# Kernel tuning notes

Hardware: AMD Instinct MI355X
Metric: run time of the kernel (lower is better)

Reference implementation:

```python
import jax, jax.numpy as jnp
import numpy as np

B, S, E, H = 8, 1024, 64, 8
DK = E // H  # n_wires per head
DIM = 2 ** DK  # statevector size


def _quantum_projection(x, phi):
    """Faithful batched simulation of _QLayer for every (batch, seq, head).
    Encoder RX(x_i) followed by trainable RX(phi_i) on the same wire equals
    RX(x_i + phi_i). Then a CNOT ring, then <Z_w> for each wire.
    x: [B,S,E] float, phi: [H,DK] float -> [B,S,E] float expectations.
    """
    b, s, e = x.shape
    theta = x.reshape(b, s, H, DK) + phi  # [B,S,H,DK]
    M = b * s * H
    th = theta.reshape(M, DK)
    # RX(t)|0> = cos(t/2)|0> - i sin(t/2)|1>
    c = jnp.cos(th * 0.5).astype(jnp.complex64)
    sn = (jnp.sin(th * 0.5) * (-1j)).astype(jnp.complex64)
    q = jnp.stack([c, sn], axis=-1)  # [M, DK, 2]
    # product state via iterated kron over the DK wires (fixed small loop)
    amps = jnp.ones((M, 1), jnp.complex64)
    for w in range(DK):
        amps = (amps[:, :, None] * q[:, w, None, :]).reshape(M, -1)
    st = amps.reshape((M,) + (2,) * DK)
    # CNOT ring: (0,1),(1,2),...,(DK-2,DK-1),(DK-1,0)
    gates = [(w, w + 1) for w in range(DK - 1)] + [(DK - 1, 0)]
    for cw, tw in gates:
        ac = 1 + cw
        s0 = jnp.take(st, 0, axis=ac)  # control = 0: identity
        s1 = jnp.take(st, 1, axis=ac)  # control = 1: flip target
        at = 1 + tw - (1 if tw > cw else 0)  # target axis after removing control axis
        s1 = jnp.flip(s1, axis=at)
        st = jnp.stack([s0, s1], axis=ac)
    stf = st.reshape(M, DIM)
    probs = stf.real ** 2 + stf.imag ** 2  # [M, DIM]
    # <Z_w> = sum_k probs[k] * (1 - 2*bit_w(k)); wire 0 is most-significant bit
    bits = (jnp.arange(DIM)[:, None] >> jnp.arange(DK - 1, -1, -1)[None, :]) & 1
    signs = (1 - 2 * bits).astype(probs.dtype)  # [DIM, DK]
    expz = probs @ signs  # [M, DK]
    return expz.reshape(b, s, e)


def setup_inputs() -> dict:
    key = jax.random.key(0)
    k1, k2, k3, k4 = jax.random.split(key, 4)
    x = jax.random.normal(k1, (B, S, E), dtype=jnp.float32)
    phi = jax.random.normal(k2, (H, DK), dtype=jnp.float32) * 0.1  # trainable RX params
    lim = 1.0 / np.sqrt(E)
    W = jax.random.uniform(k3, (E, E), jnp.float32, -lim, lim)  # combine Linear weight
    b = jax.random.uniform(k4, (E,), jnp.float32, -lim, lim)    # combine Linear bias
    return {"x": x, "phi": phi, "W": W, "b": b}


def reference(x, phi, W, b):
    # q = k = v = _projection(x): the original calls _projection(x) 3 times with
    # the same params and no randomness, so they are identical; compute once.
    proj = _quantum_projection(x, phi)  # [B,S,E]
    scores = jax.nn.softmax(
        jnp.einsum('bse,bte->bst', proj, proj) / jnp.sqrt(jnp.float32(DK)), axis=-1)
    # dropout is identity in eval mode
    ctx = jnp.einsum('bst,bte->bse', scores, proj)
    return ctx @ W.T + b
```

## Files before the change

### kernel.cpp

```cpp
#include <hip/hip_runtime.h>
#include <hip/hip_bf16.h>

#define BB 8
#define SS 1024
#define EE 64
#define HH 8
#define DKW 8

typedef __hip_bfloat16 bf16;
typedef unsigned short u16;
typedef _Float16 half8v __attribute__((ext_vector_type(8)));
typedef float floatx4 __attribute__((ext_vector_type(4)));

#define MFMA16(a, b, c) __builtin_amdgcn_mfma_f32_16x16x32_f16(a, b, c, 0, 0, 0)

#define OFF_PROJT ((size_t)BB * SS * EE * 2)

template <int NT>
__device__ __forceinline__ bool detect_f32(const u16* __restrict__ base,
                                           int tid, int* red) {
    int cnt = 0;
    for (int i = tid; i < 2048; i += NT) {
        u16 u = base[i * 2];
        int ex = (u >> 7) & 0xFF;
        cnt += (ex >= 0x84) ? 1 : 0;
    }
#pragma unroll
    for (int off = 32; off > 0; off >>= 1) cnt += __shfl_xor(cnt, off, 64);
    if ((tid & 63) == 0) red[tid >> 6] = cnt;
    __syncthreads();
    int tot = 0;
#pragma unroll
    for (int w = 0; w < NT / 64; ++w) tot += red[w];
    return tot > 64;
}

__device__ __forceinline__ void proj_compute(const void* x, const void* phi,
                                             bool f32, int m, float* z) {
    int h = m & (HH - 1);
    float th[DKW];
    if (f32) {
        const float4* xp = (const float4*)((const float*)x + (size_t)m * DKW);
        const float4* pp = (const float4*)((const float*)phi + h * DKW);
        float4 x0 = xp[0], x1 = xp[1];
        float4 p0 = pp[0], p1 = pp[1];
        th[0] = x0.x + p0.x; th[1] = x0.y + p0.y; th[2] = x0.z + p0.z; th[3] = x0.w + p0.w;
        th[4] = x1.x + p1.x; th[5] = x1.y + p1.y; th[6] = x1.z + p1.z; th[7] = x1.w + p1.w;
    } else {
        union { uint4 u; bf16 hv[8]; } xu, pu;
        xu.u = *(const uint4*)((const bf16*)x + (size_t)m * DKW);
        pu.u = *(const uint4*)((const bf16*)phi + (size_t)h * DKW);
#pragma unroll
        for (int j = 0; j < DKW; ++j)
            th[j] = __bfloat162float(xu.hv[j]) + __bfloat162float(pu.hv[j]);
    }
    float c[DKW];
#pragma unroll
    for (int j = 0; j < DKW; ++j) c[j] = __cosf(th[j]);
    float suf = c[1];
#pragma unroll
    for (int j = 2; j < DKW; ++j) suf *= c[j];
    z[0] = suf;
    float pre = c[0];
#pragma unroll
    for (int w = 1; w < DKW; ++w) { pre *= c[w]; z[w] = pre; }
}

__global__ __launch_bounds__(256) void proj_f16_kernel(const void* __restrict__ x,
                                                       const void* __restrict__ phi,
                                                       _Float16* __restrict__ projH,
                                                       _Float16* __restrict__ projT) {
    __shared__ int redd[4];
    __shared__ _Float16 zt[EE][40];
    const int tid = threadIdx.x;
    const bool f32 = detect_f32<256>((const u16*)x, tid, redd);

    const int m = blockIdx.x * 256 + tid;
    float z[DKW];
    proj_compute(x, phi, f32, m, z);

    union { half8v v; _Float16 h[8]; } o;
#pragma unroll
    for (int j = 0; j < DKW; ++j) o.h[j] = (_Float16)z[j];
    *(half8v*)(projH + (size_t)m * DKW) = o.v;

    const int h = m & (HH - 1);
    const int sl = (tid >> 3) & 31;
#pragma unroll
    for (int j = 0; j < DKW; ++j) zt[h * DKW + j][sl] = o.h[j];
    __syncthreads();

    const int b = blockIdx.x >> 5;
    const int s0 = (blockIdx.x * 32) & (SS - 1);
    const int row = tid >> 2, ch = tid & 3;
    half8v vv = *(const half8v*)(&zt[row][ch * 8]);
    *(half8v*)(projT + ((size_t)(b * EE + row)) * SS + s0 + ch * 8) = vv;
}

__device__ __forceinline__ int sidx(int row, int colblk) {
    return row * 1024 + ((colblk ^ (row & 7)) << 3);
}

__global__ __launch_bounds__(512) void fused_attn(const _Float16* __restrict__ projH,
                                                  const _Float16* __restrict__ projT,
                                                  const void* __restrict__ Wp,
                                                  const void* __restrict__ biasp,
                                                  void* __restrict__ outp) {
    __shared__ _Float16 Stile[32 * 1024];
    __shared__ _Float16 ctx_lds[32][72];
    __shared__ float    rowsum[32];
    __shared__ int      redd[8];

    const int tid = threadIdx.x;
    const int wave = tid >> 6, lane = tid & 63;
    const int lr = lane & 15, quad = lane >> 4;
    const int bid = blockIdx.x;
    const int b = bid & 7;
    const int m0 = (bid >> 3) * 32;

    const bool f32 = detect_f32<512>((const u16*)Wp, tid, redd);

    const _Float16* Pb = projH + (size_t)b * SS * EE;
    const float scale = 0.35355339059327373f;

    {
        const _Float16* ar0 = Pb + (size_t)(m0 + lr) * EE;
        const _Float16* ar1 = Pb + (size_t)(m0 + 16 + lr) * EE;
        half8v a0 = *(const half8v*)(ar0 + quad * 8);
        half8v a1 = *(const half8v*)(ar0 + 32 + quad * 8);
        half8v a2 = *(const half8v*)(ar1 + quad * 8);
        half8v a3 = *(const half8v*)(ar1 + 32 + quad * 8);
#pragma unroll 2
        for (int c = 0; c < 8; ++c) {
            int n = wave * 128 + c * 16;
            const _Float16* brow = Pb + (size_t)(n + lr) * EE;
            half8v b0 = *(const half8v*)(brow + quad * 8);
            half8v b1 = *(const half8v*)(brow + 32 + quad * 8);
            floatx4 acc0 = {0.f, 0.f, 0.f, 0.f};
            floatx4 acc1 = {0.f, 0.f, 0.f, 0.f};
            acc0 = MFMA16(a0, b0, acc0);
            acc0 = MFMA16(a1, b1, acc0);
            acc1 = MFMA16(a2, b0, acc1);
            acc1 = MFMA16(a3, b1, acc1);
            int colblk = (n + lr) >> 3, cin = (n + lr) & 7;
#pragma unroll
            for (int r = 0; r < 4; ++r) {
                Stile[sidx(quad * 4 + r, colblk) + cin]      = (_Float16)(acc0[r] * scale);
                Stile[sidx(16 + quad * 4 + r, colblk) + cin] = (_Float16)(acc1[r] * scale);
            }
        }
    }
    __syncthreads();

    {
        const int row = tid >> 4, seg = tid & 15;
        half8v hv[8];
#pragma unroll
        for (int i = 0; i < 8; ++i)
            hv[i] = *(const half8v*)(&Stile[sidx(row, i * 16 + seg)]);
        float mloc = -1e30f;
#pragma unroll
        for (int i = 0; i < 8; ++i)
#pragma unroll
            for (int j = 0; j < 8; ++j) mloc = fmaxf(mloc, (float)hv[i][j]);
#pragma unroll
        for (int off = 8; off > 0; off >>= 1)
            mloc = fmaxf(mloc, __shfl_xor(mloc, off, 64));
        float lsum = 0.f;
#pragma unroll
        for (int i = 0; i < 8; ++i) {
#pragma unroll
            for (int j = 0; j < 8; ++j) {
                float e = __expf((float)hv[i][j] - mloc);
                lsum += e;
                hv[i][j] = (_Float16)(e * 256.f);
            }
        }
#pragma unroll
        for (int off = 8; off > 0; off >>= 1)
            lsum += __shfl_xor(lsum, off, 64);
        if (seg == 0) rowsum[row] = lsum;
#pragma unroll
        for (int i = 0; i < 8; ++i)
            *(half8v*)(&Stile[sidx(row, i * 16 + seg)]) = hv[i];
    }
    __syncthreads();

    const int rowg = wave >> 2, eg = wave & 3;
    {
        const int e = eg * 16 + lr;
        const _Float16* vrow = projT + ((size_t)(b * EE + e)) * SS;
        floatx4 acc = {0.f, 0.f, 0.f, 0.f};
#pragma unroll 4
        for (int k0 = 0; k0 < SS; k0 += 32) {
            half8v A = *(const half8v*)(&Stile[sidx(rowg * 16 + lr, (k0 >> 3) + quad)]);
            half8v B = *(const half8v*)(vrow + k0 + quad * 8);
            acc = MFMA16(A, B, acc);
        }
#pragma unroll
        for (int r = 0; r < 4; ++r) {
            int row_l = rowg * 16 + quad * 4 + r;
            float inv = 1.0f / (256.0f * rowsum[row_l]);
            ctx_lds[row_l][eg * 16 + lr] = (_Float16)(acc[r] * inv);
        }
    }
    __syncthreads();

    {
        const int o = eg * 16 + lr;
        half8v ca0 = *(const half8v*)(&ctx_lds[rowg * 16 + lr][quad * 8]);
        half8v ca1 = *(const half8v*)(&ctx_lds[rowg * 16 + lr][32 + quad * 8]);
        half8v wb0, wb1;
        if (f32) {
            const float* wr = (const float*)Wp + (size_t)o * EE;
            union { half8v v; _Float16 h[8]; } w0, w1;
#pragma unroll
            for (int j = 0; j < 8; ++j) {
                w0.h[j] = (_Float16)wr[quad * 8 + j];
                w1.h[j] = (_Float16)wr[32 + quad * 8 + j];
            }
            wb0 = w0.v; wb1 = w1.v;
        } else {
            const bf16* wr = (const bf16*)Wp + (size_t)o * EE;
            union { uint4 u; bf16 hv[8]; } r0, r1;
            r0.u = *(const uint4*)(wr + quad * 8);
            r1.u = *(const uint4*)(wr + 32 + quad * 8);
            union { half8v v; _Float16 h[8]; } w0, w1;
#pragma unroll
            for (int j = 0; j < 8; ++j) {
                w0.h[j] = (_Float16)__bfloat162float(r0.hv[j]);
                w1.h[j] = (_Float16)__bfloat162float(r1.hv[j]);
            }
            wb0 = w0.v; wb1 = w1.v;
        }
        floatx4 oacc = {0.f, 0.f, 0.f, 0.f};
        oacc = MFMA16(ca0, wb0, oacc);
        oacc = MFMA16(ca1, wb1, oacc);

        float bo = f32 ? ((const float*)biasp)[o]
                       : __bfloat162float(((const bf16*)biasp)[o]);
#pragma unroll
        for (int r = 0; r < 4; ++r) {
            size_t oi = ((size_t)b * SS + m0 + rowg * 16 + quad * 4 + r) * EE + o;
            float val = oacc[r] + bo;
            if (f32) ((float*)outp)[oi] = val;
            else     ((bf16*)outp)[oi] = __float2bfloat16(val);
        }
    }
}

extern "C" void kernel_launch(void* const* d_in, const int* in_sizes, int n_in,
                              void* d_out, int out_size, void* d_ws, size_t ws_size,
                              hipStream_t stream) {
    const void* x    = d_in[0];
    const void* phi  = d_in[1];
    const void* W    = d_in[2];
    const void* bias = d_in[3];

    _Float16* projH = (_Float16*)d_ws;
    _Float16* projT = (_Float16*)((char*)d_ws + OFF_PROJT);

    proj_f16_kernel<<<dim3(BB * SS * HH / 256), dim3(256), 0, stream>>>(x, phi, projH, projT);
    fused_attn<<<dim3(256), dim3(512), 0, stream>>>(projH, projT, W, bias, d_out);
}
```

Measured before the change: 82.86 us.

## Split PV GEMM over K halves to reuse V loads, hoist W loads

The P·V stage now splits the 1024-long key dimension between two wave groups. Each wave computes both 16-row halves of the 32-row tile, so every V fragment loaded from global memory feeds two MFMAs instead of one, which halves global V traffic per block. The partial sums from the second half are combined through a new LDS buffer and an extra barrier. The W and bias loads and their conversion are hoisted to the kernel start so their latency overlaps the earlier stages, at the cost of more live registers.

```diff
diff --git a/kernel.cpp b/kernel.cpp
--- a/kernel.cpp
+++ b/kernel.cpp
@@ -107,6 +107,7 @@
                                                   const void* __restrict__ biasp,
                                                   void* __restrict__ outp) {
     __shared__ _Float16 Stile[32 * 1024];
+    __shared__ float    pacc[4][32][17];
     __shared__ _Float16 ctx_lds[32][72];
     __shared__ float    rowsum[32];
     __shared__ int      redd[8];
@@ -119,6 +120,36 @@
     const int m0 = (bid >> 3) * 32;
 
     const bool f32 = detect_f32<512>((const u16*)Wp, tid, redd);
+
+    const int o_out = (wave & 3) * 16 + lr;
+    half8v wb0, wb1;
+    float bo;
+    {
+        if (f32) {
+            const float* wr = (const float*)Wp + (size_t)o_out * EE;
+            union { half8v v; _Float16 h[8]; } w0, w1;
+#pragma unroll
+            for (int j = 0; j < 8; ++j) {
+                w0.h[j] = (_Float16)wr[quad * 8 + j];
+                w1.h[j] = (_Float16)wr[32 + quad * 8 + j];
+            }
+            wb0 = w0.v; wb1 = w1.v;
+            bo = ((const float*)biasp)[o_out];
+        } else {
+            const bf16* wr = (const bf16*)Wp + (size_t)o_out * EE;
+            union { uint4 u; bf16 hv[8]; } r0, r1;
+            r0.u = *(const uint4*)(wr + quad * 8);
+            r1.u = *(const uint4*)(wr + 32 + quad * 8);
+            union { half8v v; _Float16 h[8]; } w0, w1;
+#pragma unroll
+            for (int j = 0; j < 8; ++j) {
+                w0.h[j] = (_Float16)__bfloat162float(r0.hv[j]);
+                w1.h[j] = (_Float16)__bfloat162float(r1.hv[j]);
+            }
+            wb0 = w0.v; wb1 = w1.v;
+            bo = __bfloat162float(((const bf16*)biasp)[o_out]);
+        }
+    }
 
     const _Float16* Pb = projH + (size_t)b * SS * EE;
     const float scale = 0.35355339059327373f;
@@ -186,62 +217,52 @@
     }
     __syncthreads();
 
-    const int rowg = wave >> 2, eg = wave & 3;
+    const int kh = wave >> 2, eg = wave & 3;
     {
         const int e = eg * 16 + lr;
-        const _Float16* vrow = projT + ((size_t)(b * EE + e)) * SS;
-        floatx4 acc = {0.f, 0.f, 0.f, 0.f};
+        const _Float16* vrow = projT + ((size_t)(b * EE + e)) * SS + kh * 512;
+        floatx4 acc0 = {0.f, 0.f, 0.f, 0.f};
+        floatx4 acc1 = {0.f, 0.f, 0.f, 0.f};
 #pragma unroll 4
-        for (int k0 = 0; k0 < SS; k0 += 32) {
-            half8v A = *(const half8v*)(&Stile[sidx(rowg * 16 + lr, (k0 >> 3) + quad)]);
-            half8v B = *(const half8v*)(vrow + k0 + quad * 8);
-            acc = MFMA16(A, B, acc);
-        }
-#pragma unroll
-        for (int r = 0; r < 4; ++r) {
-            int row_l = rowg * 16 + quad * 4 + r;
-            float inv = 1.0f / (256.0f * rowsum[row_l]);
-            ctx_lds[row_l][eg * 16 + lr] = (_Float16)(acc[r] * inv);
-        }
-    }
-    __syncthreads();
-
-    {
-        const int o = eg * 16 + lr;
+        for (int k0 = 0; k0 < 512; k0 += 32) {
+            int kb = ((kh * 512 + k0) >> 3) + quad;
+            half8v B  = *(const half8v*)(vrow + k0 + quad * 8);
+            half8v A0 = *(const half8v*)(&Stile[sidx(lr, kb)]);
+            half8v A1 = *(const half8v*)(&Stile[sidx(16 + lr, kb)]);
+            acc0 = MFMA16(A0, B, acc0);
+            acc1 = MFMA16(A1, B, acc1);
+        }
+        if (kh == 1) {
+#pragma unroll
+            for (int r = 0; r < 4; ++r) {
+                pacc[eg][quad * 4 + r][lr]      = acc0[r];
+                pacc[eg][16 + quad * 4 + r][lr] = acc1[r];
+            }
+        }
+        __syncthreads();
+        if (kh == 0) {
+#pragma unroll
+            for (int r = 0; r < 4; ++r) {
+                int r0 = quad * 4 + r, r1 = 16 + quad * 4 + r;
+                float inv0 = 1.0f / (256.0f * rowsum[r0]);
+                float inv1 = 1.0f / (256.0f * rowsum[r1]);
+                ctx_lds[r0][e] = (_Float16)((acc0[r] + pacc[eg][r0][lr]) * inv0);
+                ctx_lds[r1][e] = (_Float16)((acc1[r] + pacc[eg][r1][lr]) * inv1);
+            }
+        }
+    }
+    __syncthreads();
+
+    {
+        const int rowg = wave >> 2;
         half8v ca0 = *(const half8v*)(&ctx_lds[rowg * 16 + lr][quad * 8]);
         half8v ca1 = *(const half8v*)(&ctx_lds[rowg * 16 + lr][32 + quad * 8]);
-        half8v wb0, wb1;
-        if (f32) {
-            const float* wr = (const float*)Wp + (size_t)o * EE;
-            union { half8v v; _Float16 h[8]; } w0, w1;
-#pragma unroll
-            for (int j = 0; j < 8; ++j) {
-                w0.h[j] = (_Float16)wr[quad * 8 + j];
-                w1.h[j] = (_Float16)wr[32 + quad * 8 + j];
-            }
-            wb0 = w0.v; wb1 = w1.v;
-        } else {
-            const bf16* wr = (const bf16*)Wp + (size_t)o * EE;
-            union { uint4 u; bf16 hv[8]; } r0, r1;
-            r0.u = *(const uint4*)(wr + quad * 8);
-            r1.u = *(const uint4*)(wr + 32 + quad * 8);
-            union { half8v v; _Float16 h[8]; } w0, w1;
-#pragma unroll
-            for (int j = 0; j < 8; ++j) {
-                w0.h[j] = (_Float16)__bfloat162float(r0.hv[j]);
-                w1.h[j] = (_Float16)__bfloat162float(r1.hv[j]);
-            }
-            wb0 = w0.v; wb1 = w1.v;
-        }
         floatx4 oacc = {0.f, 0.f, 0.f, 0.f};
         oacc = MFMA16(ca0, wb0, oacc);
         oacc = MFMA16(ca1, wb1, oacc);
-
-        float bo = f32 ? ((const float*)biasp)[o]
-                       : __bfloat162float(((const bf16*)biasp)[o]);
 #pragma unroll
         for (int r = 0; r < 4; ++r) {
-            size_t oi = ((size_t)b * SS + m0 + rowg * 16 + quad * 4 + r) * EE + o;
+            size_t oi = ((size_t)b * SS + m0 + rowg * 16 + quad * 4 + r) * EE + o_out;
             float val = oacc[r] + bo;
             if (f32) ((float*)outp)[oi] = val;
             else     ((bf16*)outp)[oi] = __float2bfloat16(val);
```

Result: faster. 78.43 us (median of 2 runs) (-5.3%).
